# Optimization experiments

Measured on AMD Instinct MI355X. Metric: run time of the kernel, lower is better.

The kernel has to match this reference:

```python
import jax, jax.numpy as jnp
import numpy as np

V, E, H, B, T = 50000, 256, 512, 64, 2048

def setup_inputs() -> dict:
    key = jax.random.key(0)
    ks = jax.random.split(key, 16)
    s = lambda *shp: 1.0 / np.sqrt(shp[-1])
    emb = jax.random.normal(ks[0], (V, E), dtype=jnp.float32) * 0.02
    emb = emb.at[0].set(0.0)  # padding_idx=0 row zeroed
    inp = {
        "input_token": jax.random.randint(ks[1], (B,), 0, V),
        "hidden": jax.random.normal(ks[2], (1, B, H), dtype=jnp.float32),
        "cell": jax.random.normal(ks[3], (1, B, H), dtype=jnp.float32),
        "encoder_outputs": jax.random.normal(ks[4], (B, T, H), dtype=jnp.float32),
        "emb": emb,
        "W_enc": jax.random.normal(ks[5], (H, H), dtype=jnp.float32) * s(H, H),
        "W_dec": jax.random.normal(ks[6], (H, H), dtype=jnp.float32) * s(H, H),
        "v_attn": jax.random.normal(ks[7], (H,), dtype=jnp.float32) * s(H),
        "W_ih": jax.random.normal(ks[8], (4 * H, E + H), dtype=jnp.float32) * s(4 * H, E + H),
        "W_hh": jax.random.normal(ks[9], (4 * H, H), dtype=jnp.float32) * s(4 * H, H),
        "b_ih": jax.random.normal(ks[10], (4 * H,), dtype=jnp.float32) * 0.01,
        "b_hh": jax.random.normal(ks[11], (4 * H,), dtype=jnp.float32) * 0.01,
        "W_out": jax.random.normal(ks[12], (V, 2 * H), dtype=jnp.float32) * s(V, 2 * H),
        "b_out": jnp.zeros((V,), dtype=jnp.float32),
    }
    return inp

def reference(input_token, hidden, cell, encoder_outputs, emb, W_enc, W_dec,
              v_attn, W_ih, W_hh, b_ih, b_hh, W_out, b_out):
    h = hidden[0]  # (B,H)
    c = cell[0]    # (B,H)
    # embedding lookup (dropout is identity at eval)
    embedded = emb[input_token]  # (B,E)
    # Bahdanau attention
    energy = jnp.tanh(encoder_outputs @ W_enc.T + (h @ W_dec.T)[:, None, :])  # (B,T,H)
    scores = energy @ v_attn  # (B,T)
    attn = jax.nn.softmax(scores, axis=1)
    context = jnp.einsum('bt,bth->bh', attn, encoder_outputs)  # (B,H)
    # single-step LSTM (PyTorch gate order: i, f, g, o)
    x = jnp.concatenate([embedded, context], axis=1)  # (B,E+H)
    gates = x @ W_ih.T + b_ih + h @ W_hh.T + b_hh  # (B,4H)
    i_g, f_g, g_g, o_g = jnp.split(gates, 4, axis=1)
    i_g = jax.nn.sigmoid(i_g)
    f_g = jax.nn.sigmoid(f_g)
    g_g = jnp.tanh(g_g)
    o_g = jax.nn.sigmoid(o_g)
    c_new = f_g * c + i_g * g_g
    h_new = o_g * jnp.tanh(c_new)
    # output projection
    logits = jnp.concatenate([h_new, context], axis=1) @ W_out.T + b_out  # (B,V)
    return logits, h_new[None], c_new[None], attn
```

## Files before the change

### kernel.cpp

```cpp
#include <hip/hip_runtime.h>

#define V_SZ 50000
#define E_SZ 256
#define H_SZ 512
#define B_SZ 64
#define T_SZ 2048

#define H_OFF    (B_SZ * V_SZ)
#define C_OFF    (H_OFF + B_SZ * H_SZ)
#define ATTN_OFF (C_OFF + B_SZ * H_SZ)

#define WS_X    0
#define WS_HW   (WS_X + B_SZ * 768)
#define WS_SC   (WS_HW + B_SZ * H_SZ)
#define WS_CTXP (WS_SC + B_SZ * T_SZ)
#define WS_X2   (WS_CTXP + 16 * B_SZ * H_SZ)
#define WS_GP   (WS_X2 + B_SZ * 1024)
#define WS_WB   (WS_GP + 8 * B_SZ * 2048)

typedef __attribute__((ext_vector_type(8))) short bf16x8;
typedef __attribute__((ext_vector_type(4))) float floatx4;

__device__ __forceinline__ float fast_tanh(float x) {
    return 1.f - 2.f / (__expf(2.f * x) + 1.f);
}
__device__ __forceinline__ float fast_sigmoid(float x) {
    return 1.f / (1.f + __expf(-x));
}
__device__ __forceinline__ unsigned short f2bf(float f) {
    union { float f; unsigned u; } v; v.f = f;
    unsigned r = v.u + 0x7FFFu + ((v.u >> 16) & 1u);
    return (unsigned short)(r >> 16);
}

__device__ __forceinline__ bf16x8 cvt8(float4 a, float4 b) {
    union { unsigned u[4]; bf16x8 v; } r;
    asm("v_cvt_pk_bf16_f32 %0, %1, %2" : "=v"(r.u[0]) : "v"(a.x), "v"(a.y));
    asm("v_cvt_pk_bf16_f32 %0, %1, %2" : "=v"(r.u[1]) : "v"(a.z), "v"(a.w));
    asm("v_cvt_pk_bf16_f32 %0, %1, %2" : "=v"(r.u[2]) : "v"(b.x), "v"(b.y));
    asm("v_cvt_pk_bf16_f32 %0, %1, %2" : "=v"(r.u[3]) : "v"(b.z), "v"(b.w));
    return r.v;
}

__device__ __forceinline__ void async_copy16(void* lds, const void* g) {
    __builtin_amdgcn_global_load_lds(
        (const __attribute__((address_space(1))) unsigned int*)g,
        (__attribute__((address_space(3))) unsigned int*)lds, 16, 0, 0);
}

__global__ void k0_wenc_bf16(const float* __restrict__ W_enc, float* __restrict__ ws) {
    unsigned short* Wb = (unsigned short*)(ws + WS_WB);
    const int id = blockIdx.x * 256 + threadIdx.x;
    const int j = id >> 6, kc = id & 63;
    const int k = kc * 8;
    float4 a = *(const float4*)(W_enc + j * 512 + k);
    float4 b4 = *(const float4*)(W_enc + j * 512 + k + 4);
    ushort4 lo = {f2bf(a.x), f2bf(a.y), f2bf(a.z), f2bf(a.w)};
    ushort4 hi = {f2bf(b4.x), f2bf(b4.y), f2bf(b4.z), f2bf(b4.w)};
    const int s = kc >> 2, q = kc & 3;
    const int u = 4 * j + ((q + j) & 3);
    unsigned short* dst = Wb + s * 16384 + u * 8;
    *(ushort4*)(dst) = lo;
    *(ushort4*)(dst + 4) = hi;
}

__global__ void k1_embed_hw(const int* __restrict__ tok, const float* __restrict__ hidden,
                            const float* __restrict__ emb, const float* __restrict__ W_dec,
                            float* __restrict__ ws) {
    const int b = blockIdx.x, tid = threadIdx.x;
    __shared__ __align__(16) float sh[512];
    sh[tid]       = hidden[b * 512 + tid];
    sh[tid + 256] = hidden[b * 512 + tid + 256];
    const int t = tok[b];
    ws[WS_X + b * 768 + tid] = emb[t * 256 + tid];
    __syncthreads();
    for (int jr = tid; jr < 512; jr += 256) {
        const float* w = W_dec + jr * 512;
        float acc = 0.f;
        #pragma unroll 8
        for (int k = 0; k < 512; k += 4) {
            float4 wv = *(const float4*)(w + k);
            float4 hv = *(const float4*)(sh + k);
            acc += wv.x * hv.x + wv.y * hv.y + wv.z * hv.z + wv.w * hv.w;
        }
        ws[WS_HW + b * 512 + jr] = acc;
    }
}

__global__ __launch_bounds__(256, 2)
void k2_scores(const float* __restrict__ enc, const float* __restrict__ v_attn,
               float* __restrict__ ws) {
    __shared__ __align__(16) unsigned char lds[81920];
    char* ldsB = (char*)lds;
    char* ldsA = (char*)lds + 65536;
    float* spf = (float*)lds;
    const unsigned short* Wb = (const unsigned short*)(ws + WS_WB);
    const int tid = threadIdx.x;
    const int lane = tid & 63, wv = tid >> 6;
    const int lane15 = lane & 15, quad = lane >> 4;
    const int t0 = blockIdx.x * 64, b = blockIdx.y;
    const int wn = wv * 128;
    const float* encA = enc + (size_t)(b * 2048 + t0) * 512;

    const int j0 = wn + lane15;
    const int rdBase = 64 * j0 + 16 * ((quad + j0) & 3);

    floatx4 acc[4][8];
    #pragma unroll
    for (int mt = 0; mt < 4; mt++)
        #pragma unroll
        for (int nt = 0; nt < 8; nt++) acc[mt][nt] = (floatx4){0.f, 0.f, 0.f, 0.f};

    auto stage = [&](int buf, int slice) {
        #pragma unroll
        for (int q8 = 0; q8 < 2; ++q8) {
            int f = tid + 256 * q8;
            int row = f >> 3, ul = f & 7;
            int kq = ul ^ (row & 7);
            async_copy16(ldsA + buf * 8192 + f * 16,
                         (const char*)(encA + (size_t)row * 512 + slice * 32 + kq * 4));
        }
        const char* gsB = (const char*)(Wb + slice * 16384);
        #pragma unroll
        for (int q8 = 0; q8 < 8; ++q8)
            async_copy16(ldsB + buf * 32768 + q8 * 4096 + tid * 16, gsB + q8 * 4096 + tid * 16);
    };

    auto compute = [&](int buf) {
        const char* bA = ldsA + buf * 8192;
        const char* bB = ldsB + buf * 32768;
        bf16x8 af[4];
        #pragma unroll
        for (int mt = 0; mt < 4; ++mt) {
            int row = mt * 16 + lane15, x = row & 7;
            float4 lo = *(const float4*)(bA + row * 128 + (((2 * quad) ^ x) * 16));
            float4 hi = *(const float4*)(bA + row * 128 + (((2 * quad + 1) ^ x) * 16));
            af[mt] = cvt8(lo, hi);
        }
        #pragma unroll
        for (int nt = 0; nt < 8; ++nt) {
            bf16x8 bfr = *(const bf16x8*)(bB + rdBase + nt * 1024);
            #pragma unroll
            for (int mt = 0; mt < 4; ++mt)
                acc[mt][nt] = __builtin_amdgcn_mfma_f32_16x16x32_bf16(af[mt], bfr, acc[mt][nt], 0, 0, 0);
        }
    };

    stage(0, 0);
    __syncthreads();
    for (int t = 0; t < 16; ++t) {
        if (t < 15) stage((t + 1) & 1, t + 1);
        __builtin_amdgcn_sched_barrier(0);
        compute(t & 1);
        __syncthreads();
    }

    float vj[8], hwj[8];
    #pragma unroll
    for (int nt = 0; nt < 8; nt++) {
        int jg = wn + nt * 16 + lane15;
        vj[nt] = v_attn[jg];
        hwj[nt] = ws[WS_HW + b * 512 + jg];
    }
    #pragma unroll
    for (int mt = 0; mt < 4; mt++) {
        #pragma unroll
        for (int reg = 0; reg < 4; reg++) {
            int row = mt * 16 + quad * 4 + reg;
            float s = 0.f;
            #pragma unroll
            for (int nt = 0; nt < 8; nt++)
                s += vj[nt] * fast_tanh(acc[mt][nt][reg] + hwj[nt]);
            #pragma unroll
            for (int off = 8; off; off >>= 1) s += __shfl_xor(s, off);
            if (lane15 == 0) spf[wv * 64 + row] = s;
        }
    }
    __syncthreads();
    if (tid < 64)
        ws[WS_SC + b * 2048 + t0 + tid] = spf[tid] + spf[64 + tid] + spf[128 + tid] + spf[192 + tid];
}

__global__ void k3_softmax(const float* __restrict__ ws, float* __restrict__ out) {
    const int b = blockIdx.x, tid = threadIdx.x;
    const float* s0 = ws + WS_SC + b * 2048;
    float sv[8];
    float m = -1e30f;
    #pragma unroll
    for (int i = 0; i < 8; i++) {
        int t = tid + 256 * i;
        sv[i] = s0[t];
        m = fmaxf(m, sv[i]);
    }
    #pragma unroll
    for (int o = 32; o; o >>= 1) m = fmaxf(m, __shfl_xor(m, o, 64));
    __shared__ float red[4], red2[4];
    if ((tid & 63) == 0) red[tid >> 6] = m;
    __syncthreads();
    m = fmaxf(fmaxf(red[0], red[1]), fmaxf(red[2], red[3]));
    float sum = 0.f;
    #pragma unroll
    for (int i = 0; i < 8; i++) { sv[i] = __expf(sv[i] - m); sum += sv[i]; }
    #pragma unroll
    for (int o = 32; o; o >>= 1) sum += __shfl_xor(sum, o, 64);
    if ((tid & 63) == 0) red2[tid >> 6] = sum;
    __syncthreads();
    sum = red2[0] + red2[1] + red2[2] + red2[3];
    const float inv = 1.f / sum;
    #pragma unroll
    for (int i = 0; i < 8; i++) {
        int t = tid + 256 * i;
        out[ATTN_OFF + b * 2048 + t] = sv[i] * inv;
    }
}

__global__ void k4_ctx(const float* __restrict__ enc, const float* __restrict__ attn_out,
                       float* __restrict__ ws) {
    const int ts = blockIdx.x, b = blockIdx.y, tid = threadIdx.x;
    const float* attn = attn_out + ATTN_OFF + b * 2048 + ts * 128;
    const float* ep = enc + (size_t)(b * 2048 + ts * 128) * 512 + tid * 2;
    float2 acc = {0.f, 0.f};
    #pragma unroll 4
    for (int tt = 0; tt < 128; tt++) {
        float a = attn[tt];
        float2 e = *(const float2*)(ep + (size_t)tt * 512);
        acc.x += a * e.x;
        acc.y += a * e.y;
    }
    *(float2*)(ws + WS_CTXP + (ts * 64 + b) * 512 + tid * 2) = acc;
}

__global__ void k4b_ctx_reduce(float* __restrict__ ws) {
    const int idx = blockIdx.x * 256 + threadIdx.x;
    const int b = idx >> 9, h = idx & 511;
    float s = 0.f;
    #pragma unroll
    for (int c = 0; c < 16; c++) s += ws[WS_CTXP + c * (B_SZ * 512) + b * 512 + h];
    ws[WS_X + b * 768 + 256 + h] = s;
    ws[WS_X2 + b * 1024 + 512 + h] = s;
}

__global__ __launch_bounds__(256, 2)
void k5_gates(const float* __restrict__ hidden, const float* __restrict__ W_ih,
              const float* __restrict__ W_hh, float* __restrict__ ws) {
    __shared__ __align__(16) float Wg[128 * 12];
    __shared__ __align__(16) float Zs[64 * 8];
    const int tid = threadIdx.x;
    const int jb = tid & 31, tg = tid >> 5;
    const int g0 = blockIdx.x * 128;
    const int kc = blockIdx.y;
    const int kbase = kc * 160;
    const float* xp = ws + WS_X;

    float acc[8][4];
    #pragma unroll
    for (int r = 0; r < 8; r++)
        #pragma unroll
        for (int j = 0; j < 4; j++) acc[r][j] = 0.f;

    for (int kt0 = 0; kt0 < 160; kt0 += 8) {
        const int kt = kbase + kt0;
        __syncthreads();
        {
            int row = tid >> 1, kq = tid & 1;
            int k = kt + kq * 4;
            const float* src = (k < 768) ? (W_ih + (g0 + row) * 768 + k)
                                         : (W_hh + (g0 + row) * 512 + (k - 768));
            *(float4*)(Wg + row * 12 + kq * 4) = *(const float4*)src;
        }
        if (tid < 128) {
            int row = tid >> 1, kq = tid & 1;
            int k = kt + kq * 4;
            const float* src = (k < 768) ? (xp + row * 768 + k)
                                         : (hidden + row * 512 + (k - 768));
            *(float4*)(Zs + row * 8 + kq * 4) = *(const float4*)src;
        }
        __syncthreads();

        float er[8][8];
        #pragma unroll
        for (int r = 0; r < 8; r++) {
            float4 a = *(const float4*)(Zs + (tg * 8 + r) * 8);
            float4 c = *(const float4*)(Zs + (tg * 8 + r) * 8 + 4);
            er[r][0] = a.x; er[r][1] = a.y; er[r][2] = a.z; er[r][3] = a.w;
            er[r][4] = c.x; er[r][5] = c.y; er[r][6] = c.z; er[r][7] = c.w;
        }
        #pragma unroll
        for (int jj = 0; jj < 4; jj++) {
            const float* wr = Wg + (jb + 32 * jj) * 12;
            float4 w0 = *(const float4*)(wr);
            float4 w1 = *(const float4*)(wr + 4);
            float w[8] = {w0.x, w0.y, w0.z, w0.w, w1.x, w1.y, w1.z, w1.w};
            #pragma unroll
            for (int r = 0; r < 8; r++)
                #pragma unroll
                for (int k = 0; k < 8; k++) acc[r][jj] += er[r][k] * w[k];
        }
    }
    #pragma unroll
    for (int jj = 0; jj < 4; jj++)
        #pragma unroll
        for (int r = 0; r < 8; r++)
            ws[WS_GP + kc * (B_SZ * 2048) + (tg * 8 + r) * 2048 + g0 + jb + 32 * jj] = acc[r][jj];
}

__global__ void k5b_lstm(const float* __restrict__ cell, const float* __restrict__ b_ih,
                         const float* __restrict__ b_hh, float* __restrict__ ws,
                         float* __restrict__ out) {
    const int e = blockIdx.x * 256 + threadIdx.x;
    const int b = e >> 9, hh = e & 511;
    float g4[4];
    #pragma unroll
    for (int q = 0; q < 4; q++) {
        float s = b_ih[q * 512 + hh] + b_hh[q * 512 + hh];
        #pragma unroll
        for (int c = 0; c < 8; c++)
            s += ws[WS_GP + c * (B_SZ * 2048) + b * 2048 + q * 512 + hh];
        g4[q] = s;
    }
    const float ig = fast_sigmoid(g4[0]);
    const float fg = fast_sigmoid(g4[1]);
    const float gg = fast_tanh(g4[2]);
    const float og = fast_sigmoid(g4[3]);
    const float c_old = cell[b * 512 + hh];
    const float c_new = fg * c_old + ig * gg;
    const float h_new = og * fast_tanh(c_new);
    out[H_OFF + b * 512 + hh] = h_new;
    out[C_OFF + b * 512 + hh] = c_new;
    ws[WS_X2 + b * 1024 + hh] = h_new;
}

__global__ __launch_bounds__(256, 3)
void k6_logits(const float* __restrict__ W_out, const float* __restrict__ b_out,
               const float* __restrict__ ws, float* __restrict__ out) {
    __shared__ __align__(16) unsigned char lds[49152];
    char* ldsW = (char*)lds;
    char* ldsX = (char*)lds + 32768;
    const float* x2f = ws + WS_X2;
    const int tid = threadIdx.x;
    const int lane = tid & 63, wv = tid >> 6;
    const int lane15 = lane & 15, quad = lane >> 4;
    const int v0 = blockIdx.x * 128;
    const int wn = wv * 32;

    floatx4 acc[4][2];
    #pragma unroll
    for (int mt = 0; mt < 4; mt++)
        #pragma unroll
        for (int nt = 0; nt < 2; nt++) acc[mt][nt] = (floatx4){0.f, 0.f, 0.f, 0.f};

    auto stage = [&](int buf, int slice) {
        #pragma unroll
        for (int q8 = 0; q8 < 2; ++q8) {
            int f = tid + 256 * q8;
            int row = f >> 3, ul = f & 7;
            int kq = ul ^ (row & 7);
            async_copy16(ldsX + buf * 8192 + f * 16,
                         (const char*)(x2f + row * 1024 + slice * 32 + kq * 4));
        }
        #pragma unroll
        for (int q8 = 0; q8 < 4; ++q8) {
            int f = tid + 256 * q8;
            int row = f >> 3, ul = f & 7;
            int v = v0 + row; if (v > V_SZ - 1) v = V_SZ - 1;
            int kq = ul ^ (row & 7);
            async_copy16(ldsW + buf * 16384 + f * 16,
                         (const char*)(W_out + (size_t)v * 1024 + slice * 32 + kq * 4));
        }
    };

    auto compute = [&](int buf) {
        const char* bX = ldsX + buf * 8192;
        const char* bW = ldsW + buf * 16384;
        bf16x8 af[4];
        #pragma unroll
        for (int mt = 0; mt < 4; ++mt) {
            int row = mt * 16 + lane15, x = row & 7;
            float4 lo = *(const float4*)(bX + row * 128 + (((2 * quad) ^ x) * 16));
            float4 hi = *(const float4*)(bX + row * 128 + (((2 * quad + 1) ^ x) * 16));
            af[mt] = cvt8(lo, hi);
        }
        #pragma unroll
        for (int nt = 0; nt < 2; ++nt) {
            int row = wn + nt * 16 + lane15, x = row & 7;
            float4 lo = *(const float4*)(bW + row * 128 + (((2 * quad) ^ x) * 16));
            float4 hi = *(const float4*)(bW + row * 128 + (((2 * quad + 1) ^ x) * 16));
            bf16x8 bfr = cvt8(lo, hi);
            #pragma unroll
            for (int mt = 0; mt < 4; ++mt)
                acc[mt][nt] = __builtin_amdgcn_mfma_f32_16x16x32_bf16(af[mt], bfr, acc[mt][nt], 0, 0, 0);
        }
    };

    stage(0, 0);
    __syncthreads();
    for (int t = 0; t < 32; ++t) {
        if (t < 31) stage((t + 1) & 1, t + 1);
        __builtin_amdgcn_sched_barrier(0);
        compute(t & 1);
        __syncthreads();
    }

    #pragma unroll
    for (int nt = 0; nt < 2; nt++) {
        const int v = v0 + wn + nt * 16 + lane15;
        if (v < V_SZ) {
            const float bo = b_out[v];
            #pragma unroll
            for (int mt = 0; mt < 4; mt++)
                #pragma unroll
                for (int reg = 0; reg < 4; reg++) {
                    const int br = mt * 16 + quad * 4 + reg;
                    out[br * V_SZ + v] = acc[mt][nt][reg] + bo;
                }
        }
    }
}

extern "C" void kernel_launch(void* const* d_in, const int* in_sizes, int n_in,
                              void* d_out, int out_size, void* d_ws, size_t ws_size,
                              hipStream_t stream) {
    (void)in_sizes; (void)n_in; (void)out_size; (void)ws_size;
    const int*   tok    = (const int*)d_in[0];
    const float* hidden = (const float*)d_in[1];
    const float* cell   = (const float*)d_in[2];
    const float* enc    = (const float*)d_in[3];
    const float* emb    = (const float*)d_in[4];
    const float* W_enc  = (const float*)d_in[5];
    const float* W_dec  = (const float*)d_in[6];
    const float* v_attn = (const float*)d_in[7];
    const float* W_ih   = (const float*)d_in[8];
    const float* W_hh   = (const float*)d_in[9];
    const float* b_ih   = (const float*)d_in[10];
    const float* b_hh   = (const float*)d_in[11];
    const float* W_out  = (const float*)d_in[12];
    const float* b_out  = (const float*)d_in[13];
    float* out = (float*)d_out;
    float* ws  = (float*)d_ws;

    k0_wenc_bf16<<<dim3(128), dim3(256), 0, stream>>>(W_enc, ws);
    k1_embed_hw<<<dim3(64), dim3(256), 0, stream>>>(tok, hidden, emb, W_dec, ws);
    k2_scores<<<dim3(32, 64), dim3(256), 0, stream>>>(enc, v_attn, ws);
    k3_softmax<<<dim3(64), dim3(256), 0, stream>>>(ws, out);
    k4_ctx<<<dim3(16, 64), dim3(256), 0, stream>>>(enc, out, ws);
    k4b_ctx_reduce<<<dim3(128), dim3(256), 0, stream>>>(ws);
    k5_gates<<<dim3(16, 8), dim3(256), 0, stream>>>(hidden, W_ih, W_hh, ws);
    k5b_lstm<<<dim3(128), dim3(256), 0, stream>>>(cell, b_ih, b_hh, ws, out);
    k6_logits<<<dim3(391), dim3(256), 0, stream>>>(W_out, b_out, ws, out);
}
```

Measured before the change: 685.7 us.

## Preload full encoder tile as bf16 in LDS, halve logits tile size

The scores kernel now loads the whole 64x512 encoder tile once, converts it to bf16 and keeps it resident in a 64KB LDS region, so only the W_enc slices are streamed through the double buffer. It also changes the W_enc swizzle to reduce LDS bank conflicts. The logits kernel halves its tile to 64 vocab rows per block, doubling the grid and raising occupancy to 4 blocks per CU. The trade-off is 128KB of LDS per block in k2, which limits occupancy and gives up async overlap on the encoder loads.

```diff
diff --git a/kernel.cpp b/kernel.cpp
--- a/kernel.cpp
+++ b/kernel.cpp
@@ -58,7 +58,7 @@
     ushort4 lo = {f2bf(a.x), f2bf(a.y), f2bf(a.z), f2bf(a.w)};
     ushort4 hi = {f2bf(b4.x), f2bf(b4.y), f2bf(b4.z), f2bf(b4.w)};
     const int s = kc >> 2, q = kc & 3;
-    const int u = 4 * j + ((q + j) & 3);
+    const int u = 4 * j + ((q + (j >> 1)) & 3);
     unsigned short* dst = Wb + s * 16384 + u * 8;
     *(ushort4*)(dst) = lo;
     *(ushort4*)(dst + 4) = hi;
@@ -90,10 +90,10 @@
 __global__ __launch_bounds__(256, 2)
 void k2_scores(const float* __restrict__ enc, const float* __restrict__ v_attn,
                float* __restrict__ ws) {
-    __shared__ __align__(16) unsigned char lds[81920];
-    char* ldsB = (char*)lds;
-    char* ldsA = (char*)lds + 65536;
-    float* spf = (float*)lds;
+    __shared__ __align__(16) unsigned char lds[131072];
+    char* ldsA = (char*)lds;
+    char* ldsB = (char*)lds + 65536;
+    float* spf = (float*)(lds + 65536);
     const unsigned short* Wb = (const unsigned short*)(ws + WS_WB);
     const int tid = threadIdx.x;
     const int lane = tid & 63, wv = tid >> 6;
@@ -103,55 +103,54 @@
     const float* encA = enc + (size_t)(b * 2048 + t0) * 512;
 
     const int j0 = wn + lane15;
-    const int rdBase = 64 * j0 + 16 * ((quad + j0) & 3);
-
-    floatx4 acc[4][8];
-    #pragma unroll
-    for (int mt = 0; mt < 4; mt++)
-        #pragma unroll
-        for (int nt = 0; nt < 8; nt++) acc[mt][nt] = (floatx4){0.f, 0.f, 0.f, 0.f};
-
-    auto stage = [&](int buf, int slice) {
-        #pragma unroll
-        for (int q8 = 0; q8 < 2; ++q8) {
-            int f = tid + 256 * q8;
-            int row = f >> 3, ul = f & 7;
-            int kq = ul ^ (row & 7);
-            async_copy16(ldsA + buf * 8192 + f * 16,
-                         (const char*)(encA + (size_t)row * 512 + slice * 32 + kq * 4));
-        }
+    const int rdBase = 64 * j0 + 16 * ((quad + (j0 >> 1)) & 3);
+
+    auto stageB = [&](int buf, int slice) {
         const char* gsB = (const char*)(Wb + slice * 16384);
         #pragma unroll
         for (int q8 = 0; q8 < 8; ++q8)
             async_copy16(ldsB + buf * 32768 + q8 * 4096 + tid * 16, gsB + q8 * 4096 + tid * 16);
     };
 
-    auto compute = [&](int buf) {
-        const char* bA = ldsA + buf * 8192;
-        const char* bB = ldsB + buf * 32768;
-        bf16x8 af[4];
-        #pragma unroll
-        for (int mt = 0; mt < 4; ++mt) {
-            int row = mt * 16 + lane15, x = row & 7;
-            float4 lo = *(const float4*)(bA + row * 128 + (((2 * quad) ^ x) * 16));
-            float4 hi = *(const float4*)(bA + row * 128 + (((2 * quad + 1) ^ x) * 16));
-            af[mt] = cvt8(lo, hi);
-        }
-        #pragma unroll
-        for (int nt = 0; nt < 8; ++nt) {
-            bf16x8 bfr = *(const bf16x8*)(bB + rdBase + nt * 1024);
-            #pragma unroll
-            for (int mt = 0; mt < 4; ++mt)
-                acc[mt][nt] = __builtin_amdgcn_mfma_f32_16x16x32_bf16(af[mt], bfr, acc[mt][nt], 0, 0, 0);
-        }
-    };
-
-    stage(0, 0);
-    __syncthreads();
+    #pragma unroll
+    for (int u = 0; u < 16; ++u) {
+        int g = u * 256 + tid;
+        int row = g >> 6, ku = g & 63;
+        const float* src = encA + (size_t)row * 512 + ku * 8;
+        float4 lo = *(const float4*)src;
+        float4 hi = *(const float4*)(src + 4);
+        bf16x8 v8 = cvt8(lo, hi);
+        *(bf16x8*)(ldsA + row * 1024 + ((ku ^ (row & 7)) * 16)) = v8;
+    }
+    stageB(0, 0);
+    __syncthreads();
+
+    floatx4 acc[4][8];
+    #pragma unroll
+    for (int mt = 0; mt < 4; mt++)
+        #pragma unroll
+        for (int nt = 0; nt < 8; nt++) acc[mt][nt] = (floatx4){0.f, 0.f, 0.f, 0.f};
+
     for (int t = 0; t < 16; ++t) {
-        if (t < 15) stage((t + 1) & 1, t + 1);
+        if (t < 15) stageB((t + 1) & 1, t + 1);
         __builtin_amdgcn_sched_barrier(0);
-        compute(t & 1);
+        {
+            const char* bB = ldsB + (t & 1) * 32768;
+            bf16x8 af[4];
+            #pragma unroll
+            for (int mt = 0; mt < 4; ++mt) {
+                int row = mt * 16 + lane15;
+                int c = t * 4 + quad;
+                af[mt] = *(const bf16x8*)(ldsA + row * 1024 + ((c ^ (row & 7)) * 16));
+            }
+            #pragma unroll
+            for (int nt = 0; nt < 8; ++nt) {
+                bf16x8 bfr = *(const bf16x8*)(bB + rdBase + nt * 1024);
+                #pragma unroll
+                for (int mt = 0; mt < 4; ++mt)
+                    acc[mt][nt] = __builtin_amdgcn_mfma_f32_16x16x32_bf16(af[mt], bfr, acc[mt][nt], 0, 0, 0);
+            }
+        }
         __syncthreads();
     }
 
@@ -330,24 +329,22 @@
     ws[WS_X2 + b * 1024 + hh] = h_new;
 }
 
-__global__ __launch_bounds__(256, 3)
+__global__ __launch_bounds__(256, 4)
 void k6_logits(const float* __restrict__ W_out, const float* __restrict__ b_out,
                const float* __restrict__ ws, float* __restrict__ out) {
-    __shared__ __align__(16) unsigned char lds[49152];
+    __shared__ __align__(16) unsigned char lds[32768];
     char* ldsW = (char*)lds;
-    char* ldsX = (char*)lds + 32768;
+    char* ldsX = (char*)lds + 16384;
     const float* x2f = ws + WS_X2;
     const int tid = threadIdx.x;
     const int lane = tid & 63, wv = tid >> 6;
     const int lane15 = lane & 15, quad = lane >> 4;
-    const int v0 = blockIdx.x * 128;
-    const int wn = wv * 32;
-
-    floatx4 acc[4][2];
-    #pragma unroll
-    for (int mt = 0; mt < 4; mt++)
-        #pragma unroll
-        for (int nt = 0; nt < 2; nt++) acc[mt][nt] = (floatx4){0.f, 0.f, 0.f, 0.f};
+    const int v0 = blockIdx.x * 64;
+    const int wn = wv * 16;
+
+    floatx4 acc[4];
+    #pragma unroll
+    for (int mt = 0; mt < 4; mt++) acc[mt] = (floatx4){0.f, 0.f, 0.f, 0.f};
 
     auto stage = [&](int buf, int slice) {
         #pragma unroll
@@ -359,19 +356,19 @@
                          (const char*)(x2f + row * 1024 + slice * 32 + kq * 4));
         }
         #pragma unroll
-        for (int q8 = 0; q8 < 4; ++q8) {
+        for (int q8 = 0; q8 < 2; ++q8) {
             int f = tid + 256 * q8;
             int row = f >> 3, ul = f & 7;
             int v = v0 + row; if (v > V_SZ - 1) v = V_SZ - 1;
             int kq = ul ^ (row & 7);
-            async_copy16(ldsW + buf * 16384 + f * 16,
+            async_copy16(ldsW + buf * 8192 + f * 16,
                          (const char*)(W_out + (size_t)v * 1024 + slice * 32 + kq * 4));
         }
     };
 
     auto compute = [&](int buf) {
         const char* bX = ldsX + buf * 8192;
-        const char* bW = ldsW + buf * 16384;
+        const char* bW = ldsW + buf * 8192;
         bf16x8 af[4];
         #pragma unroll
         for (int mt = 0; mt < 4; ++mt) {
@@ -380,15 +377,14 @@
             float4 hi = *(const float4*)(bX + row * 128 + (((2 * quad + 1) ^ x) * 16));
             af[mt] = cvt8(lo, hi);
         }
-        #pragma unroll
-        for (int nt = 0; nt < 2; ++nt) {
-            int row = wn + nt * 16 + lane15, x = row & 7;
+        {
+            int row = wn + lane15, x = row & 7;
             float4 lo = *(const float4*)(bW + row * 128 + (((2 * quad) ^ x) * 16));
             float4 hi = *(const float4*)(bW + row * 128 + (((2 * quad + 1) ^ x) * 16));
             bf16x8 bfr = cvt8(lo, hi);
             #pragma unroll
             for (int mt = 0; mt < 4; ++mt)
-                acc[mt][nt] = __builtin_amdgcn_mfma_f32_16x16x32_bf16(af[mt], bfr, acc[mt][nt], 0, 0, 0);
+                acc[mt] = __builtin_amdgcn_mfma_f32_16x16x32_bf16(af[mt], bfr, acc[mt], 0, 0, 0);
         }
     };
 
@@ -401,9 +397,8 @@
         __syncthreads();
     }
 
-    #pragma unroll
-    for (int nt = 0; nt < 2; nt++) {
-        const int v = v0 + wn + nt * 16 + lane15;
+    {
+        const int v = v0 + wn + lane15;
         if (v < V_SZ) {
             const float bo = b_out[v];
             #pragma unroll
@@ -411,7 +406,7 @@
                 #pragma unroll
                 for (int reg = 0; reg < 4; reg++) {
                     const int br = mt * 16 + quad * 4 + reg;
-                    out[br * V_SZ + v] = acc[mt][nt][reg] + bo;
+                    out[br * V_SZ + v] = acc[mt][reg] + bo;
                 }
         }
     }
@@ -446,5 +441,5 @@
     k4b_ctx_reduce<<<dim3(128), dim3(256), 0, stream>>>(ws);
     k5_gates<<<dim3(16, 8), dim3(256), 0, stream>>>(hidden, W_ih, W_hh, ws);
     k5b_lstm<<<dim3(128), dim3(256), 0, stream>>>(cell, b_ih, b_hh, ws, out);
-    k6_logits<<<dim3(391), dim3(256), 0, stream>>>(W_out, b_out, ws, out);
-}
+    k6_logits<<<dim3(782), dim3(256), 0, stream>>>(W_out, b_out, ws, out);
+}
```

Result: slower. 787.4 us (+14.8%).
